# Kernel tuning notes

Hardware: AMD Instinct MI355X
Metric: run time of the kernel (lower is better)

Reference implementation:

```python
import jax, jax.numpy as jnp
import numpy as np

N_NODES = 16384
N_EDGES = 98304
N_CAND = 1024
# GAT config from default __init__: heads=[8,8,1], features=[3,64,128,64]
LAYERS = [
    (3, 8, 64, True, True),      # (f_in, n_heads, f_out, concat, elu)
    (512, 8, 128, True, True),
    (1024, 1, 64, False, False),
]


def _gat_layer(x, src, tgt, W, a_src, a_tgt, b, skipW, nh, fo, concat, act):
    n = x.shape[0]
    proj = (x @ W).reshape(n, nh, fo)                 # [N, NH, F]
    s_src = jnp.einsum('nhf,hf->nh', proj, a_src)     # [N, NH]
    s_tgt = jnp.einsum('nhf,hf->nh', proj, a_tgt)
    e = jax.nn.leaky_relu(s_src[src] + s_tgt[tgt], 0.2)   # [E, NH]
    # numerically stable segment softmax over incoming edges of each target node
    e_max = jax.ops.segment_max(e, tgt, num_segments=n)
    ex = jnp.exp(e - jax.lax.stop_gradient(e_max)[tgt])
    denom = jax.ops.segment_sum(ex, tgt, num_segments=n)
    alpha = ex / (denom[tgt] + 1e-16)                 # [E, NH]
    agg = jax.ops.segment_sum(proj[src] * alpha[:, :, None], tgt, num_segments=n)
    out = agg + (x @ skipW).reshape(n, nh, fo)        # skip connection (projected)
    out = out.reshape(n, nh * fo) if concat else out.mean(axis=1)
    out = out + b
    return jax.nn.elu(out) if act else out


def setup_inputs() -> dict:
    key = jax.random.key(0)
    ks = iter(jax.random.split(key, 32))
    d = {}
    d['fea'] = jax.random.normal(next(ks), (N_NODES, 3), dtype=jnp.float32)
    d['edge_index'] = jax.random.randint(next(ks), (2, N_EDGES), 0, N_NODES, dtype=jnp.int32)
    d['candidates_id'] = jax.random.randint(next(ks), (N_CAND,), 0, N_NODES, dtype=jnp.int32)
    for i, (fi, nh, fo, concat, _) in enumerate(LAYERS):
        sc = 1.0 / np.sqrt(fi)
        d[f'W{i}'] = jax.random.normal(next(ks), (fi, nh * fo), dtype=jnp.float32) * sc
        d[f'a_src{i}'] = jax.random.normal(next(ks), (nh, fo), dtype=jnp.float32) * 0.1
        d[f'a_tgt{i}'] = jax.random.normal(next(ks), (nh, fo), dtype=jnp.float32) * 0.1
        d[f'b{i}'] = jnp.zeros((nh * fo if concat else fo,), dtype=jnp.float32)
        d[f'skip{i}'] = jax.random.normal(next(ks), (fi, nh * fo), dtype=jnp.float32) * sc
    # MLP head build_mlp(256, 3, 64, 1): 64->256 Tanh 256->256 Tanh 256->1
    for j, (a, bdim) in enumerate([(64, 256), (256, 256), (256, 1)], start=1):
        d[f'mW{j}'] = jax.random.normal(next(ks), (a, bdim), dtype=jnp.float32) / np.sqrt(a)
        d[f'mb{j}'] = jnp.zeros((bdim,), dtype=jnp.float32)
    return d


def reference(fea, edge_index, candidates_id,
              W0, a_src0, a_tgt0, b0, skip0,
              W1, a_src1, a_tgt1, b1, skip1,
              W2, a_src2, a_tgt2, b2, skip2,
              mW1, mb1, mW2, mb2, mW3, mb3):
    src, tgt = edge_index[0], edge_index[1]
    x = fea
    params = [(W0, a_src0, a_tgt0, b0, skip0), (W1, a_src1, a_tgt1, b1, skip1),
              (W2, a_src2, a_tgt2, b2, skip2)]
    for (fi, nh, fo, concat, act), (W, asr, atg, b, sk) in zip(LAYERS, params):
        x = _gat_layer(x, src, tgt, W, asr, atg, b, sk, nh, fo, concat, act)
    cand = x[candidates_id]                              # [C, 64]
    h = jnp.tanh(cand @ mW1 + mb1)
    h = jnp.tanh(h @ mW2 + mb2)
    prob = (h @ mW3 + mb3).squeeze(-1)                   # [C]
    return prob, candidates_id
```

## Files before the change

### kernel.cpp

```cpp
#include <hip/hip_runtime.h>
#include <cmath>

#define N_NODES 16384
#define N_EDGES 98304
#define N_CAND  1024

typedef __bf16 bf16x8 __attribute__((ext_vector_type(8)));
typedef short  s16x8  __attribute__((ext_vector_type(8)));
typedef float  f32x4  __attribute__((ext_vector_type(4)));
typedef unsigned short u16x2 __attribute__((ext_vector_type(2)));
typedef unsigned short u16x4 __attribute__((ext_vector_type(4)));

__device__ __forceinline__ unsigned short f2bf(float x) {
    unsigned u = __float_as_uint(x);
    return (unsigned short)((u + 0x7fffu + ((u >> 16) & 1u)) >> 16);
}
__device__ __forceinline__ float bf2f(unsigned short b) {
    return __uint_as_float((unsigned)b << 16);
}

#define GLL(gp, lp) __builtin_amdgcn_global_load_lds(                          \
    (const __attribute__((address_space(1))) unsigned int*)(const void*)(gp),  \
    (__attribute__((address_space(3))) unsigned int*)(void*)(lp), 16, 0, 0)

__global__ __launch_bounds__(256) void k_hist(const int* __restrict__ tgt,
                                              int* __restrict__ deg) {
    int e = blockIdx.x * 256 + threadIdx.x;
    if (e < N_EDGES) atomicAdd(&deg[tgt[e]], 1);
}

__global__ __launch_bounds__(256) void k_scan_all(const int* __restrict__ deg,
                                                  int* __restrict__ off,
                                                  int* __restrict__ cursor) {
    __shared__ int ts[256];
    int tid = threadIdx.x;
    const int4* d4 = (const int4*)(deg + tid * 64);
    int s = 0;
    #pragma unroll
    for (int i = 0; i < 16; ++i) {
        int4 v = d4[i];
        s += v.x + v.y + v.z + v.w;
    }
    ts[tid] = s;
    __syncthreads();
    for (int o = 1; o < 256; o <<= 1) {
        int t = (tid >= o) ? ts[tid - o] : 0;
        __syncthreads();
        ts[tid] += t;
        __syncthreads();
    }
    int run = ts[tid] - s;
    int4* o4 = (int4*)(off + tid * 64);
    int4* c4 = (int4*)(cursor + tid * 64);
    #pragma unroll
    for (int i = 0; i < 16; ++i) {
        int4 v = d4[i];
        int4 ov;
        ov.x = run; run += v.x;
        ov.y = run; run += v.y;
        ov.z = run; run += v.z;
        ov.w = run; run += v.w;
        o4[i] = ov;
        c4[i] = ov;
    }
    if (tid == 255) off[N_NODES] = run;
}

__global__ __launch_bounds__(256) void k_scatter(const int* __restrict__ ei,
                                                 int* __restrict__ cursor,
                                                 int* __restrict__ csrc) {
    int e = blockIdx.x * 256 + threadIdx.x;
    if (e < N_EDGES) {
        int s = ei[e];
        int t = ei[N_EDGES + e];
        int pos = atomicAdd(&cursor[t], 1);
        csrc[pos] = s;
    }
}

__global__ __launch_bounds__(256) void k_l0s(const float* __restrict__ fea,
                                             const float* __restrict__ W0,
                                             const float* __restrict__ as,
                                             const float* __restrict__ at,
                                             float* __restrict__ ssrc,
                                             float* __restrict__ stgt) {
    int n = blockIdx.x, tid = threadIdx.x;
    float f0 = fea[n * 3 + 0], f1 = fea[n * 3 + 1], f2 = fea[n * 3 + 2];
    int c1 = tid, c2 = tid + 256;
    float p1 = f0 * W0[c1] + f1 * W0[512 + c1] + f2 * W0[1024 + c1];
    float p2 = f0 * W0[c2] + f1 * W0[512 + c2] + f2 * W0[1024 + c2];
    float vs1 = p1 * as[c1], vt1 = p1 * at[c1];
    float vs2 = p2 * as[c2], vt2 = p2 * at[c2];
    #pragma unroll
    for (int o = 32; o; o >>= 1) {
        vs1 += __shfl_xor(vs1, o); vt1 += __shfl_xor(vt1, o);
        vs2 += __shfl_xor(vs2, o); vt2 += __shfl_xor(vt2, o);
    }
    int lane = tid & 63, w = tid >> 6;
    if (lane == 0) {
        ssrc[n * 8 + w]     = vs1;  stgt[n * 8 + w]     = vt1;
        ssrc[n * 8 + w + 4] = vs2;  stgt[n * 8 + w + 4] = vt2;
    }
}

__device__ __forceinline__ void pack_slot(const float* __restrict__ src0,
                                          const float* __restrict__ src1,
                                          int splitN, int NTOT, int NKB, int s,
                                          unsigned short* __restrict__ hi,
                                          unsigned short* __restrict__ lo) {
    int nb = s / (NKB * 512);
    int rem = s - nb * (NKB * 512);
    int kb = rem >> 9;
    int sl = rem & 511;
    int c = sl >> 7, n = sl & 127;
    int col = nb * 128 + n;
    const float* src;
    int cc, stride;
    if (col < splitN) { src = src0; cc = col; stride = splitN; }
    else              { src = src1; cc = col - splitN; stride = NTOT - splitN; }
    int k0 = kb * 32 + c * 8;
    s16x8 hv, lv;
    #pragma unroll
    for (int j = 0; j < 8; ++j) {
        float w = src[(size_t)(k0 + j) * stride + cc];
        unsigned short h = f2bf(w);
        hv[j] = (short)h;
        lv[j] = (short)f2bf(w - bf2f(h));
    }
    *(s16x8*)(hi + (size_t)s * 8) = hv;
    *(s16x8*)(lo + (size_t)s * 8) = lv;
}

__global__ __launch_bounds__(256) void k_pack_all(
    const float* __restrict__ W1, const float* __restrict__ sk1,
    unsigned short* __restrict__ pw1h, unsigned short* __restrict__ pw1l,
    const float* __restrict__ W2, const float* __restrict__ sk2,
    unsigned short* __restrict__ pw2h, unsigned short* __restrict__ pw2l) {
    int s = blockIdx.x * 256 + threadIdx.x;
    if (s < 131072) {
        pack_slot(W1, sk1, 1024, 2048, 16, s, pw1h, pw1l);
    } else {
        int s2 = s - 131072;
        if (s2 < 16384) pack_slot(W2, sk2, 64, 128, 32, s2, pw2h, pw2l);
    }
}

template <int F, int NTOT, int KS>
__global__ __launch_bounds__(256, 2) void k_gemm_mfma(
    const unsigned short* __restrict__ Xhi, const unsigned short* __restrict__ Xlo,
    const unsigned short* __restrict__ Wph, const unsigned short* __restrict__ Wpl,
    float* __restrict__ out0, float* __restrict__ out1, int splitN) {
    constexpr int NKB = F / 32;
    static_assert(KS == 1 || NTOT == 128, "split-K assumes single col-block");
    __shared__ unsigned short lds[2 * 16384];
    const int tid = threadIdx.x;
    const int bm  = blockIdx.y * 128;
    const int nb  = blockIdx.x;

    const int sA0 = tid, sA1 = tid + 256;
    const int rA0 = sA0 >> 2, rA1 = sA1 >> 2;
    const int cA0 = (sA0 & 3) ^ ((rA0 >> 1) & 3);
    const int cA1 = (sA1 & 3) ^ ((rA1 >> 1) & 3);
    const unsigned short* gAh0 = Xhi + (size_t)(bm + rA0) * F + cA0 * 8;
    const unsigned short* gAh1 = Xhi + (size_t)(bm + rA1) * F + cA1 * 8;
    const unsigned short* gAl0 = Xlo + (size_t)(bm + rA0) * F + cA0 * 8;
    const unsigned short* gAl1 = Xlo + (size_t)(bm + rA1) * F + cA1 * 8;
    const unsigned short* gBh  = Wph + (KS == 1 ? (size_t)nb * NKB * 4096 : 0);
    const unsigned short* gBl  = Wpl + (KS == 1 ? (size_t)nb * NKB * 4096 : 0);

    const int wave = tid >> 6, lane = tid & 63;
    const int wm = wave >> 1, wn = wave & 1;
    const int l15 = lane & 15, lc = lane >> 4;

    int offA[4], offB[4];
    #pragma unroll
    for (int mi = 0; mi < 4; ++mi) {
        int row = wm * 64 + mi * 16 + l15;
        int chp = lc ^ ((row >> 1) & 3);
        offA[mi] = row * 32 + chp * 8;
    }
    #pragma unroll
    for (int ni = 0; ni < 4; ++ni) {
        int n = wn * 64 + ni * 16 + l15;
        offB[ni] = 8192 + (lc * 128 + n) * 8;
    }

    f32x4 acc[4][4];
    #pragma unroll
    for (int i = 0; i < 4; ++i)
        #pragma unroll
        for (int j = 0; j < 4; ++j)
            acc[i][j] = (f32x4){0.f, 0.f, 0.f, 0.f};

    auto stage = [&](int kb, int buf) {
        unsigned short* l = &lds[buf * 16384];
        const size_t ka  = (size_t)kb * 32;
        const size_t kbb = (size_t)kb * 4096;
        GLL(gAh0 + ka, l + sA0 * 8);
        GLL(gAh1 + ka, l + sA1 * 8);
        GLL(gAl0 + ka, l + 4096 + sA0 * 8);
        GLL(gAl1 + ka, l + 4096 + sA1 * 8);
        GLL(gBh + kbb + sA0 * 8, l + 8192 + sA0 * 8);
        GLL(gBh + kbb + sA1 * 8, l + 8192 + sA1 * 8);
        GLL(gBl + kbb + sA0 * 8, l + 12288 + sA0 * 8);
        GLL(gBl + kbb + sA1 * 8, l + 12288 + sA1 * 8);
    };

    const int kb0 = (KS > 1) ? nb * (NKB / KS) : 0;
    const int kbN = (KS > 1) ? (NKB / KS) : NKB;

    stage(kb0, 0);
    __syncthreads();

    for (int ki = 0; ki < kbN; ++ki) {
        const int buf = ki & 1;
        if (ki + 1 < kbN) stage(kb0 + ki + 1, buf ^ 1);
        const unsigned short* l = &lds[buf * 16384];
        bf16x8 ah[4], al[4], bh[4], bl[4];
        #pragma unroll
        for (int mi = 0; mi < 4; ++mi) {
            ah[mi] = *(const bf16x8*)(l + offA[mi]);
            al[mi] = *(const bf16x8*)(l + 4096 + offA[mi]);
        }
        #pragma unroll
        for (int ni = 0; ni < 4; ++ni) {
            bh[ni] = *(const bf16x8*)(l + offB[ni]);
            bl[ni] = *(const bf16x8*)(l + 4096 + offB[ni]);
        }
        #pragma unroll
        for (int mi = 0; mi < 4; ++mi)
            #pragma unroll
            for (int ni = 0; ni < 4; ++ni) {
                acc[mi][ni] = __builtin_amdgcn_mfma_f32_16x16x32_bf16(ah[mi], bh[ni], acc[mi][ni], 0, 0, 0);
                acc[mi][ni] = __builtin_amdgcn_mfma_f32_16x16x32_bf16(ah[mi], bl[ni], acc[mi][ni], 0, 0, 0);
                acc[mi][ni] = __builtin_amdgcn_mfma_f32_16x16x32_bf16(al[mi], bh[ni], acc[mi][ni], 0, 0, 0);
            }
        __syncthreads();
    }

    if constexpr (KS > 1) {
        #pragma unroll
        for (int ni = 0; ni < 4; ++ni) {
            int col = wn * 64 + ni * 16 + l15;
            #pragma unroll
            for (int mi = 0; mi < 4; ++mi) {
                int row0 = bm + wm * 64 + mi * 16 + lc * 4;
                #pragma unroll
                for (int r = 0; r < 4; ++r)
                    out0[((size_t)nb * N_NODES + row0 + r) * NTOT + col] = acc[mi][ni][r];
            }
        }
    } else {
        #pragma unroll
        for (int ni = 0; ni < 4; ++ni) {
            int col = nb * 128 + wn * 64 + ni * 16 + l15;
            float* o;
            int cc, stride;
            if (col < splitN) { o = out0; cc = col; stride = splitN; }
            else              { o = out1; cc = col - splitN; stride = NTOT - splitN; }
            #pragma unroll
            for (int mi = 0; mi < 4; ++mi) {
                int row0 = bm + wm * 64 + mi * 16 + lc * 4;
                #pragma unroll
                for (int r = 0; r < 4; ++r)
                    o[(size_t)(row0 + r) * stride + cc] = acc[mi][ni][r];
            }
        }
    }
}

__global__ __launch_bounds__(256) void k_red2s(const float* __restrict__ part,
                                               const float* __restrict__ as2,
                                               const float* __restrict__ at2,
                                               float* __restrict__ P2,
                                               float* __restrict__ S2,
                                               float* __restrict__ ssrc,
                                               float* __restrict__ stgt) {
    int tid = threadIdx.x;
    int node = blockIdx.x * 16 + (tid >> 4);
    int cg = tid & 15;
    int c0 = cg * 8;
    const float* p0 = part + (size_t)node * 128 + c0;
    float v[8];
    {
        float4 a = *(const float4*)(p0);
        float4 b = *(const float4*)(p0 + 4);
        v[0]=a.x; v[1]=a.y; v[2]=a.z; v[3]=a.w; v[4]=b.x; v[5]=b.y; v[6]=b.z; v[7]=b.w;
    }
    #pragma unroll
    for (int ks = 1; ks < 4; ++ks) {
        const float* pk = p0 + (size_t)ks * N_NODES * 128;
        float4 a = *(const float4*)(pk);
        float4 b = *(const float4*)(pk + 4);
        v[0]+=a.x; v[1]+=a.y; v[2]+=a.z; v[3]+=a.w; v[4]+=b.x; v[5]+=b.y; v[6]+=b.z; v[7]+=b.w;
    }
    if (cg < 8) {
        float s = 0.f, t = 0.f;
        #pragma unroll
        for (int j = 0; j < 8; ++j) {
            s += v[j] * as2[c0 + j];
            t += v[j] * at2[c0 + j];
        }
        #pragma unroll
        for (int o = 1; o < 8; o <<= 1) { s += __shfl_xor(s, o); t += __shfl_xor(t, o); }
        float* d = P2 + (size_t)node * 64 + c0;
        *(float4*)(d)     = make_float4(v[0], v[1], v[2], v[3]);
        *(float4*)(d + 4) = make_float4(v[4], v[5], v[6], v[7]);
        if (cg == 0) { ssrc[node] = s; stgt[node] = t; }
    } else {
        float* d = S2 + (size_t)node * 64 + (c0 - 64);
        *(float4*)(d)     = make_float4(v[0], v[1], v[2], v[3]);
        *(float4*)(d + 4) = make_float4(v[4], v[5], v[6], v[7]);
    }
}

template <int H, int FO>
__global__ __launch_bounds__(256) void k_scores(const float* __restrict__ P,
                                                const float* __restrict__ asrc,
                                                const float* __restrict__ atgt,
                                                float* __restrict__ ssrc,
                                                float* __restrict__ stgt) {
    constexpr int K = H * FO;
    int gid  = blockIdx.x * 4 + (threadIdx.x >> 6);
    int lane = threadIdx.x & 63;
    int n = gid / H, h = gid - n * H;
    if (n >= N_NODES) return;
    float vs = 0.f, vt = 0.f;
    #pragma unroll
    for (int q = 0; q < FO / 64; ++q) {
        int f = lane + q * 64;
        float p = P[(size_t)n * K + h * FO + f];
        vs += p * asrc[h * FO + f];
        vt += p * atgt[h * FO + f];
    }
    #pragma unroll
    for (int o = 32; o; o >>= 1) {
        vs += __shfl_xor(vs, o);
        vt += __shfl_xor(vt, o);
    }
    if (lane == 0) {
        ssrc[n * H + h] = vs;
        stgt[n * H + h] = vt;
    }
}

__global__ __launch_bounds__(256) void k_attn0(
    const float* __restrict__ fea, const float* __restrict__ W0,
    const float* __restrict__ sk0, const float* __restrict__ ssrc,
    const float* __restrict__ stgt, const int* __restrict__ off,
    const int* __restrict__ csrc, const float* __restrict__ bias,
    unsigned short* __restrict__ ohi, unsigned short* __restrict__ olo) {
    constexpr int H = 8, K = 512;
    int n = blockIdx.x, tid = threadIdx.x;
    __shared__ float st[H], mh[H], dh[H];
    __shared__ int   srcs[256];
    __shared__ float sfea[256][3];
    __shared__ float av[256 * H];
    const int c0 = tid * 2, h0 = tid >> 5;

    float w00 = W0[c0],        w01 = W0[c0 + 1];
    float w10 = W0[512 + c0],  w11 = W0[512 + c0 + 1];
    float w20 = W0[1024 + c0], w21 = W0[1024 + c0 + 1];

    int d0 = off[n], deg = off[n + 1] - d0;
    if (tid < H) st[tid] = stgt[n * H + tid];
    __syncthreads();

    float a0 = 0.f, a1 = 0.f;

    if (deg <= 256) {
        int cnt = deg;
        if (tid < cnt) srcs[tid] = csrc[d0 + tid];
        __syncthreads();
        for (int idx = tid; idx < cnt * 3; idx += 256)
            sfea[idx / 3][idx % 3] = fea[srcs[idx / 3] * 3 + idx % 3];
        for (int idx = tid; idx < cnt * H; idx += 256) {
            int e = idx >> 3, h = idx & 7;
            float v = ssrc[srcs[e] * H + h] + st[h];
            av[idx] = (v >= 0.f) ? v : 0.2f * v;
        }
        __syncthreads();
        if (tid < H) {
            float m = -INFINITY;
            for (int e = 0; e < cnt; ++e) m = fmaxf(m, av[e * H + tid]);
            float s = 0.f;
            for (int e = 0; e < cnt; ++e) s += expf(av[e * H + tid] - m);
            mh[tid] = m;
            dh[tid] = 1.f / (s + 1e-16f);
        }
        __syncthreads();
        for (int idx = tid; idx < cnt * H; idx += 256) {
            int h = idx & 7;
            av[idx] = expf(av[idx] - mh[h]) * dh[h];
        }
        __syncthreads();
        for (int e = 0; e < cnt; ++e) {
            float al = av[e * H + h0];
            float f0 = sfea[e][0], f1 = sfea[e][1], f2 = sfea[e][2];
            a0 += (f0 * w00 + f1 * w10 + f2 * w20) * al;
            a1 += (f0 * w01 + f1 * w11 + f2 * w21) * al;
        }
    } else {
        if (tid < H) { mh[tid] = -INFINITY; dh[tid] = 0.f; }
        __syncthreads();
        for (int base = 0; base < deg; base += 256) {
            int cnt = min(256, deg - base);
            if (tid < cnt) srcs[tid] = csrc[d0 + base + tid];
            __syncthreads();
            for (int idx = tid; idx < cnt * H; idx += 256) {
                int e = idx >> 3, h = idx & 7;
                float v = ssrc[srcs[e] * H + h] + st[h];
                av[idx] = (v >= 0.f) ? v : 0.2f * v;
            }
            __syncthreads();
            if (tid < H) {
                float m = mh[tid], d = dh[tid];
                float cm = -INFINITY;
                for (int e = 0; e < cnt; ++e) cm = fmaxf(cm, av[e * H + tid]);
                float nm = fmaxf(m, cm);
                float s = 0.f;
                for (int e = 0; e < cnt; ++e) s += expf(av[e * H + tid] - nm);
                d = ((m == -INFINITY) ? 0.f : d * expf(m - nm)) + s;
                mh[tid] = nm;
                dh[tid] = d;
            }
            __syncthreads();
        }
        if (tid < H) dh[tid] = 1.f / (dh[tid] + 1e-16f);
        __syncthreads();
        for (int base = 0; base < deg; base += 256) {
            int cnt = min(256, deg - base);
            if (tid < cnt) srcs[tid] = csrc[d0 + base + tid];
            __syncthreads();
            for (int idx = tid; idx < cnt * 3; idx += 256)
                sfea[idx / 3][idx % 3] = fea[srcs[idx / 3] * 3 + idx % 3];
            for (int idx = tid; idx < cnt * H; idx += 256) {
                int e = idx >> 3, h = idx & 7;
                float v = ssrc[srcs[e] * H + h] + st[h];
                v = (v >= 0.f) ? v : 0.2f * v;
                av[idx] = expf(v - mh[h]) * dh[h];
            }
            __syncthreads();
            for (int e = 0; e < cnt; ++e) {
                float al = av[e * H + h0];
                float f0 = sfea[e][0], f1 = sfea[e][1], f2 = sfea[e][2];
                a0 += (f0 * w00 + f1 * w10 + f2 * w20) * al;
                a1 += (f0 * w01 + f1 * w11 + f2 * w21) * al;
            }
            __syncthreads();
        }
    }

    float f0 = fea[n * 3], f1 = fea[n * 3 + 1], f2 = fea[n * 3 + 2];
    float r0 = a0 + f0 * sk0[c0]     + f1 * sk0[512 + c0]     + f2 * sk0[1024 + c0]     + bias[c0];
    float r1 = a1 + f0 * sk0[c0 + 1] + f1 * sk0[512 + c0 + 1] + f2 * sk0[1024 + c0 + 1] + bias[c0 + 1];
    r0 = (r0 > 0.f) ? r0 : expm1f(r0);
    r1 = (r1 > 0.f) ? r1 : expm1f(r1);
    u16x2 hv, lv;
    unsigned short hb0 = f2bf(r0); hv[0] = hb0; lv[0] = f2bf(r0 - bf2f(hb0));
    unsigned short hb1 = f2bf(r1); hv[1] = hb1; lv[1] = f2bf(r1 - bf2f(hb1));
    *(u16x2*)(ohi + (size_t)n * K + c0) = hv;
    *(u16x2*)(olo + (size_t)n * K + c0) = lv;
}

template <int H, int FO, bool ACT, bool SPLIT>
__global__ __launch_bounds__(256) void k_attn_g(
    const float* __restrict__ P, const float* __restrict__ ssrc,
    const float* __restrict__ stgt, const int* __restrict__ off,
    const int* __restrict__ csrc, const float* __restrict__ bias,
    const float* __restrict__ skipin, float* __restrict__ outf,
    unsigned short* __restrict__ ohi, unsigned short* __restrict__ olo) {
    constexpr int K   = H * FO;
    constexpr int VEC = (K / 256 >= 4) ? 4 : ((K / 256 >= 1) ? (K / 256) : 1);
    constexpr int NT  = K / VEC;
    int n = blockIdx.x, tid = threadIdx.x;
    __shared__ float st[H], mh[H], dh[H];
    __shared__ int   srcs[256];
    __shared__ float av[256 * H];

    const int c0 = (tid < NT ? tid : 0) * VEC;
    const int h0 = c0 / FO;
    const float* pc = P + c0;

    int d0 = off[n], deg = off[n + 1] - d0;
    if (tid < H) st[tid] = stgt[n * H + tid];
    __syncthreads();

    float acc[VEC];
    #pragma unroll
    for (int j = 0; j < VEC; ++j) acc[j] = 0.f;

    if (deg <= 256) {
        int cnt = deg;
        if (tid < cnt) srcs[tid] = csrc[d0 + tid];
        __syncthreads();
        for (int idx = tid; idx < cnt * H; idx += 256) {
            int e = idx / H, h = idx - (idx / H) * H;
            float v = ssrc[srcs[e] * H + h] + st[h];
            av[idx] = (v >= 0.f) ? v : 0.2f * v;
        }
        __syncthreads();
        if (tid < H) {
            float m = -INFINITY;
            for (int e = 0; e < cnt; ++e) m = fmaxf(m, av[e * H + tid]);
            float s = 0.f;
            for (int e = 0; e < cnt; ++e) s += expf(av[e * H + tid] - m);
            mh[tid] = m;
            dh[tid] = 1.f / (s + 1e-16f);
        }
        __syncthreads();
        for (int idx = tid; idx < cnt * H; idx += 256) {
            int h = idx - (idx / H) * H;
            av[idx] = expf(av[idx] - mh[h]) * dh[h];
        }
        __syncthreads();
        if (NT == 256 || tid < NT) {
            for (int e = 0; e < cnt; ++e) {
                float a = av[e * H + h0];
                if constexpr (VEC == 4) {
                    const float4 v = *(const float4*)(pc + (size_t)srcs[e] * K);
                    acc[0] += v.x * a; acc[1] += v.y * a;
                    acc[2] += v.z * a; acc[3] += v.w * a;
                } else {
                    acc[0] += pc[(size_t)srcs[e] * K] * a;
                }
            }
        }
    } else {
        if (tid < H) { mh[tid] = -INFINITY; dh[tid] = 0.f; }
        __syncthreads();
        for (int base = 0; base < deg; base += 256) {
            int cnt = min(256, deg - base);
            if (tid < cnt) srcs[tid] = csrc[d0 + base + tid];
            __syncthreads();
            for (int idx = tid; idx < cnt * H; idx += 256) {
                int e = idx / H, h = idx - (idx / H) * H;
                float v = ssrc[srcs[e] * H + h] + st[h];
                av[idx] = (v >= 0.f) ? v : 0.2f * v;
            }
            __syncthreads();
            if (tid < H) {
                float m = mh[tid], d = dh[tid];
                float cm = -INFINITY;
                for (int e = 0; e < cnt; ++e) cm = fmaxf(cm, av[e * H + tid]);
                float nm = fmaxf(m, cm);
                float s = 0.f;
                for (int e = 0; e < cnt; ++e) s += expf(av[e * H + tid] - nm);
                d = ((m == -INFINITY) ? 0.f : d * expf(m - nm)) + s;
                mh[tid] = nm;
                dh[tid] = d;
            }
            __syncthreads();
        }
        if (tid < H) dh[tid] = 1.f / (dh[tid] + 1e-16f);
        __syncthreads();
        for (int base = 0; base < deg; base += 256) {
            int cnt = min(256, deg - base);
            if (tid < cnt) srcs[tid] = csrc[d0 + base + tid];
            __syncthreads();
            for (int idx = tid; idx < cnt * H; idx += 256) {
                int e = idx / H, h = idx - (idx / H) * H;
                float v = ssrc[srcs[e] * H + h] + st[h];
                v = (v >= 0.f) ? v : 0.2f * v;
                av[idx] = expf(v - mh[h]) * dh[h];
            }
            __syncthreads();
            if (NT == 256 || tid < NT) {
                for (int e = 0; e < cnt; ++e) {
                    float a = av[e * H + h0];
                    if constexpr (VEC == 4) {
                        const float4 v = *(const float4*)(pc + (size_t)srcs[e] * K);
                        acc[0] += v.x * a; acc[1] += v.y * a;
                        acc[2] += v.z * a; acc[3] += v.w * a;
                    } else {
                        acc[0] += pc[(size_t)srcs[e] * K] * a;
                    }
                }
            }
            __syncthreads();
        }
    }

    if (NT == 256 || tid < NT) {
        float r[VEC];
        if constexpr (VEC == 4) {
            const float4 s4 = *(const float4*)(skipin + (size_t)n * K + c0);
            r[0] = acc[0] + s4.x; r[1] = acc[1] + s4.y;
            r[2] = acc[2] + s4.z; r[3] = acc[3] + s4.w;
        } else {
            r[0] = acc[0] + skipin[(size_t)n * K + c0];
        }
        #pragma unroll
        for (int j = 0; j < VEC; ++j) {
            r[j] += bias[c0 + j];
            if (ACT) r[j] = (r[j] > 0.f) ? r[j] : expm1f(r[j]);
        }
        if constexpr (SPLIT) {
            if constexpr (VEC == 4) {
                u16x4 hv, lv;
                #pragma unroll
                for (int j = 0; j < 4; ++j) {
                    unsigned short hb = f2bf(r[j]);
                    hv[j] = hb; lv[j] = f2bf(r[j] - bf2f(hb));
                }
                *(u16x4*)(ohi + (size_t)n * K + c0) = hv;
                *(u16x4*)(olo + (size_t)n * K + c0) = lv;
            } else {
                unsigned short hb = f2bf(r[0]);
                ohi[(size_t)n * K + c0] = hb;
                olo[(size_t)n * K + c0] = f2bf(r[0] - bf2f(hb));
            }
        } else {
            if constexpr (VEC == 4) {
                *(float4*)(outf + (size_t)n * K + c0) =
                    make_float4(r[0], r[1], r[2], r[3]);
            } else {
                outf[(size_t)n * K + c0] = r[0];
            }
        }
    }
}

__global__ __launch_bounds__(256) void k_mlp(const float* __restrict__ X3,
                                             const int* __restrict__ cid,
                                             const float* __restrict__ W1,
                                             const float* __restrict__ b1,
                                             const float* __restrict__ W2,
                                             const float* __restrict__ b2,
                                             const float* __restrict__ W3,
                                             const float* __restrict__ b3,
                                             float* __restrict__ out) {
    __shared__ float cf[64], h1[256], red[4];
    int c = blockIdx.x, tid = threadIdx.x;
    int id = cid[c];
    if (tid < 64) cf[tid] = X3[(size_t)id * 64 + tid];
    __syncthreads();
    float a = b1[tid];
    #pragma unroll 8
    for (int k = 0; k < 64; ++k) a += cf[k] * W1[k * 256 + tid];
    h1[tid] = tanhf(a);
    __syncthreads();
    float a2 = b2[tid];
    #pragma unroll 8
    for (int k = 0; k < 256; ++k) a2 += h1[k] * W2[k * 256 + tid];
    float v = tanhf(a2) * W3[tid];
    #pragma unroll
    for (int o = 32; o; o >>= 1) v += __shfl_xor(v, o);
    if ((tid & 63) == 0) red[tid >> 6] = v;
    __syncthreads();
    if (tid == 0) {
        out[c] = red[0] + red[1] + red[2] + red[3] + b3[0];
        out[N_CAND + c] = (float)id;
    }
}

extern "C" void kernel_launch(void* const* d_in, const int* in_sizes, int n_in,
                              void* d_out, int out_size, void* d_ws, size_t ws_size,
                              hipStream_t stream) {
    const float* fea  = (const float*)d_in[0];
    const int*   ei   = (const int*)d_in[1];
    const int*   cid  = (const int*)d_in[2];
    const float* W0   = (const float*)d_in[3];
    const float* as0  = (const float*)d_in[4];
    const float* at0  = (const float*)d_in[5];
    const float* b0   = (const float*)d_in[6];
    const float* sk0  = (const float*)d_in[7];
    const float* W1   = (const float*)d_in[8];
    const float* as1  = (const float*)d_in[9];
    const float* at1  = (const float*)d_in[10];
    const float* b1   = (const float*)d_in[11];
    const float* sk1  = (const float*)d_in[12];
    const float* W2   = (const float*)d_in[13];
    const float* as2  = (const float*)d_in[14];
    const float* at2  = (const float*)d_in[15];
    const float* b2   = (const float*)d_in[16];
    const float* sk2  = (const float*)d_in[17];
    const float* mW1  = (const float*)d_in[18];
    const float* mb1  = (const float*)d_in[19];
    const float* mW2  = (const float*)d_in[20];
    const float* mb2  = (const float*)d_in[21];
    const float* mW3  = (const float*)d_in[22];
    const float* mb3  = (const float*)d_in[23];

    char* w = (char*)d_ws;
    auto alloc = [&](size_t bytes) -> void* {
        void* p = (void*)w;
        w += (bytes + 255) & ~(size_t)255;
        return p;
    };
    int*   deg    = (int*)alloc((size_t)N_NODES * 4);
    int*   off    = (int*)alloc((size_t)(N_NODES + 1) * 4);
    int*   cursor = (int*)alloc((size_t)N_NODES * 4);
    int*   csrc   = (int*)alloc((size_t)N_EDGES * 4);
    float* ssrc   = (float*)alloc((size_t)N_NODES * 8 * 4);
    float* stgt   = (float*)alloc((size_t)N_NODES * 8 * 4);
    float* P      = (float*)alloc((size_t)N_NODES * 1024 * 4);
    float* S      = (float*)alloc((size_t)N_NODES * 1024 * 4);
    unsigned short* Xs = (unsigned short*)alloc((size_t)N_NODES * 1024 * 4);
    unsigned short* pw1h = (unsigned short*)alloc((size_t)512 * 2048 * 2);
    unsigned short* pw1l = (unsigned short*)alloc((size_t)512 * 2048 * 2);
    unsigned short* pw2h = (unsigned short*)alloc((size_t)1024 * 128 * 2);
    unsigned short* pw2l = (unsigned short*)alloc((size_t)1024 * 128 * 2);

    unsigned short* X1hi = Xs;
    unsigned short* X1lo = Xs + (size_t)N_NODES * 512;
    unsigned short* X2hi = Xs;
    unsigned short* X2lo = Xs + (size_t)N_NODES * 1024;
    float* part = P;
    float* P2   = S;
    float* S2   = S + (size_t)N_NODES * 64;
    float* X3   = S + (size_t)2 * N_NODES * 64;

    hipMemsetAsync(deg, 0, (size_t)N_NODES * 4, stream);
    k_hist<<<N_EDGES / 256, 256, 0, stream>>>(ei + N_EDGES, deg);
    k_scan_all<<<1, 256, 0, stream>>>(deg, off, cursor);
    k_scatter<<<N_EDGES / 256, 256, 0, stream>>>(ei, cursor, csrc);

    k_pack_all<<<576, 256, 0, stream>>>(W1, sk1, pw1h, pw1l, W2, sk2, pw2h, pw2l);

    k_l0s<<<N_NODES, 256, 0, stream>>>(fea, W0, as0, at0, ssrc, stgt);
    k_attn0<<<N_NODES, 256, 0, stream>>>(fea, W0, sk0, ssrc, stgt, off, csrc,
                                         b0, X1hi, X1lo);

    {
        dim3 g(16, N_NODES / 128);
        k_gemm_mfma<512, 2048, 1><<<g, 256, 0, stream>>>(X1hi, X1lo, pw1h, pw1l, P, S, 1024);
    }
    k_scores<8, 128><<<N_NODES * 8 / 4, 256, 0, stream>>>(P, as1, at1, ssrc, stgt);
    k_attn_g<8, 128, true, true><<<N_NODES, 256, 0, stream>>>(
        P, ssrc, stgt, off, csrc, b1, S, nullptr, X2hi, X2lo);

    {
        dim3 g(4, N_NODES / 128);
        k_gemm_mfma<1024, 128, 4><<<g, 256, 0, stream>>>(X2hi, X2lo, pw2h, pw2l, part, nullptr, 128);
    }
    k_red2s<<<N_NODES / 16, 256, 0, stream>>>(part, as2, at2, P2, S2, ssrc, stgt);
    k_attn_g<1, 64, false, false><<<N_NODES, 256, 0, stream>>>(
        P2, ssrc, stgt, off, csrc, b2, S2, X3, nullptr, nullptr);

    k_mlp<<<N_CAND, 256, 0, stream>>>(X3, cid, mW1, mb1, mW2, mb2, mW3, mb3,
                                      (float*)d_out);
}
```

Measured before the change: 468.4 us.

## Fuse layer-1 scores into GEMM epilogue, compute last layer only for candidates, batch MLP

The layer-1 attention score dot products move into the MFMA GEMM epilogue, which removes the separate k_scores kernel and its re-read of the 16384x1024 projection. The final GAT layer's aggregation now runs only for the 1024 candidate nodes instead of all 16384, because only those rows are consumed by the MLP. The MLP kernel is batched to process 16 candidates per block, so W1 and W2 loads are reused across candidates. The costs are extra LDS use and a sync in the GEMM epilogue, plus higher register pressure in the MLP.

```diff
diff --git a/kernel.cpp b/kernel.cpp
--- a/kernel.cpp
+++ b/kernel.cpp
@@ -145,11 +145,13 @@
     }
 }
 
-template <int F, int NTOT, int KS>
+template <int F, int NTOT, int KS, bool FS>
 __global__ __launch_bounds__(256, 2) void k_gemm_mfma(
     const unsigned short* __restrict__ Xhi, const unsigned short* __restrict__ Xlo,
     const unsigned short* __restrict__ Wph, const unsigned short* __restrict__ Wpl,
-    float* __restrict__ out0, float* __restrict__ out1, int splitN) {
+    float* __restrict__ out0, float* __restrict__ out1, int splitN,
+    const float* __restrict__ as, const float* __restrict__ at,
+    float* __restrict__ ssrc, float* __restrict__ stgt) {
     constexpr int NKB = F / 32;
     static_assert(KS == 1 || NTOT == 128, "split-K assumes single col-block");
     __shared__ unsigned short lds[2 * 16384];
@@ -264,6 +266,44 @@
                 #pragma unroll
                 for (int r = 0; r < 4; ++r)
                     o[(size_t)(row0 + r) * stride + cc] = acc[mi][ni][r];
+            }
+        }
+        if constexpr (FS) {
+            if (nb < 8) {
+                float* sredS = (float*)lds;
+                float* sredT = sredS + 256;
+                const float* av_ = as + nb * 128;
+                const float* atv = at + nb * 128;
+                #pragma unroll
+                for (int mi = 0; mi < 4; ++mi) {
+                    #pragma unroll
+                    for (int r = 0; r < 4; ++r) {
+                        float ps = 0.f, pt = 0.f;
+                        #pragma unroll
+                        for (int ni = 0; ni < 4; ++ni) {
+                            int f = wn * 64 + ni * 16 + l15;
+                            float v = acc[mi][ni][r];
+                            ps += v * av_[f];
+                            pt += v * atv[f];
+                        }
+                        #pragma unroll
+                        for (int o = 1; o < 16; o <<= 1) {
+                            ps += __shfl_xor(ps, o);
+                            pt += __shfl_xor(pt, o);
+                        }
+                        if (l15 == 0) {
+                            int rl = wm * 64 + mi * 16 + lc * 4 + r;
+                            sredS[wn * 128 + rl] = ps;
+                            sredT[wn * 128 + rl] = pt;
+                        }
+                    }
+                }
+                __syncthreads();
+                if (tid < 128) {
+                    int row = bm + tid;
+                    ssrc[row * 8 + nb] = sredS[tid] + sredS[128 + tid];
+                    stgt[row * 8 + nb] = sredT[tid] + sredT[128 + tid];
+                }
             }
         }
     }
@@ -314,36 +354,6 @@
     }
 }
 
-template <int H, int FO>
-__global__ __launch_bounds__(256) void k_scores(const float* __restrict__ P,
-                                                const float* __restrict__ asrc,
-                                                const float* __restrict__ atgt,
-                                                float* __restrict__ ssrc,
-                                                float* __restrict__ stgt) {
-    constexpr int K = H * FO;
-    int gid  = blockIdx.x * 4 + (threadIdx.x >> 6);
-    int lane = threadIdx.x & 63;
-    int n = gid / H, h = gid - n * H;
-    if (n >= N_NODES) return;
-    float vs = 0.f, vt = 0.f;
-    #pragma unroll
-    for (int q = 0; q < FO / 64; ++q) {
-        int f = lane + q * 64;
-        float p = P[(size_t)n * K + h * FO + f];
-        vs += p * asrc[h * FO + f];
-        vt += p * atgt[h * FO + f];
-    }
-    #pragma unroll
-    for (int o = 32; o; o >>= 1) {
-        vs += __shfl_xor(vs, o);
-        vt += __shfl_xor(vt, o);
-    }
-    if (lane == 0) {
-        ssrc[n * H + h] = vs;
-        stgt[n * H + h] = vt;
-    }
-}
-
 __global__ __launch_bounds__(256) void k_attn0(
     const float* __restrict__ fea, const float* __restrict__ W0,
     const float* __restrict__ sk0, const float* __restrict__ ssrc,
@@ -463,17 +473,20 @@
     *(u16x2*)(olo + (size_t)n * K + c0) = lv;
 }
 
-template <int H, int FO, bool ACT, bool SPLIT>
+template <int H, int FO, bool ACT, bool SPLIT, bool CAND>
 __global__ __launch_bounds__(256) void k_attn_g(
     const float* __restrict__ P, const float* __restrict__ ssrc,
     const float* __restrict__ stgt, const int* __restrict__ off,
     const int* __restrict__ csrc, const float* __restrict__ bias,
     const float* __restrict__ skipin, float* __restrict__ outf,
-    unsigned short* __restrict__ ohi, unsigned short* __restrict__ olo) {
+    unsigned short* __restrict__ ohi, unsigned short* __restrict__ olo,
+    const int* __restrict__ nidx) {
     constexpr int K   = H * FO;
     constexpr int VEC = (K / 256 >= 4) ? 4 : ((K / 256 >= 1) ? (K / 256) : 1);
     constexpr int NT  = K / VEC;
-    int n = blockIdx.x, tid = threadIdx.x;
+    int n = CAND ? nidx[blockIdx.x] : blockIdx.x;
+    int orow = CAND ? blockIdx.x : n;
+    int tid = threadIdx.x;
     __shared__ float st[H], mh[H], dh[H];
     __shared__ int   srcs[256];
     __shared__ float av[256 * H];
@@ -603,25 +616,25 @@
                     unsigned short hb = f2bf(r[j]);
                     hv[j] = hb; lv[j] = f2bf(r[j] - bf2f(hb));
                 }
-                *(u16x4*)(ohi + (size_t)n * K + c0) = hv;
-                *(u16x4*)(olo + (size_t)n * K + c0) = lv;
+                *(u16x4*)(ohi + (size_t)orow * K + c0) = hv;
+                *(u16x4*)(olo + (size_t)orow * K + c0) = lv;
             } else {
                 unsigned short hb = f2bf(r[0]);
-                ohi[(size_t)n * K + c0] = hb;
-                olo[(size_t)n * K + c0] = f2bf(r[0] - bf2f(hb));
+                ohi[(size_t)orow * K + c0] = hb;
+                olo[(size_t)orow * K + c0] = f2bf(r[0] - bf2f(hb));
             }
         } else {
             if constexpr (VEC == 4) {
-                *(float4*)(outf + (size_t)n * K + c0) =
+                *(float4*)(outf + (size_t)orow * K + c0) =
                     make_float4(r[0], r[1], r[2], r[3]);
             } else {
-                outf[(size_t)n * K + c0] = r[0];
-            }
-        }
-    }
-}
-
-__global__ __launch_bounds__(256) void k_mlp(const float* __restrict__ X3,
+                outf[(size_t)orow * K + c0] = r[0];
+            }
+        }
+    }
+}
+
+__global__ __launch_bounds__(256) void k_mlp(const float* __restrict__ X3c,
                                              const int* __restrict__ cid,
                                              const float* __restrict__ W1,
                                              const float* __restrict__ b1,
@@ -630,27 +643,46 @@
                                              const float* __restrict__ W3,
                                              const float* __restrict__ b3,
                                              float* __restrict__ out) {
-    __shared__ float cf[64], h1[256], red[4];
-    int c = blockIdx.x, tid = threadIdx.x;
-    int id = cid[c];
-    if (tid < 64) cf[tid] = X3[(size_t)id * 64 + tid];
+    __shared__ float cf[16][64];
+    __shared__ float h1s[16][256];
+    __shared__ float red[16][4];
+    int tid = threadIdx.x;
+    int cbase = blockIdx.x * 16;
+    for (int i = tid; i < 16 * 64; i += 256)
+        cf[i >> 6][i & 63] = X3c[(size_t)cbase * 64 + i];
     __syncthreads();
-    float a = b1[tid];
-    #pragma unroll 8
-    for (int k = 0; k < 64; ++k) a += cf[k] * W1[k * 256 + tid];
-    h1[tid] = tanhf(a);
+    float a[16];
+    #pragma unroll
+    for (int ci = 0; ci < 16; ++ci) a[ci] = b1[tid];
+    for (int k = 0; k < 64; ++k) {
+        float wv = W1[k * 256 + tid];
+        #pragma unroll
+        for (int ci = 0; ci < 16; ++ci) a[ci] += cf[ci][k] * wv;
+    }
+    #pragma unroll
+    for (int ci = 0; ci < 16; ++ci) h1s[ci][tid] = tanhf(a[ci]);
     __syncthreads();
-    float a2 = b2[tid];
-    #pragma unroll 8
-    for (int k = 0; k < 256; ++k) a2 += h1[k] * W2[k * 256 + tid];
-    float v = tanhf(a2) * W3[tid];
-    #pragma unroll
-    for (int o = 32; o; o >>= 1) v += __shfl_xor(v, o);
-    if ((tid & 63) == 0) red[tid >> 6] = v;
+    #pragma unroll
+    for (int ci = 0; ci < 16; ++ci) a[ci] = b2[tid];
+    for (int k = 0; k < 256; ++k) {
+        float wv = W2[k * 256 + tid];
+        #pragma unroll
+        for (int ci = 0; ci < 16; ++ci) a[ci] += h1s[ci][k] * wv;
+    }
+    float w3 = W3[tid];
+    int lane = tid & 63, wv_ = tid >> 6;
+    #pragma unroll
+    for (int ci = 0; ci < 16; ++ci) {
+        float v = tanhf(a[ci]) * w3;
+        #pragma unroll
+        for (int o = 32; o; o >>= 1) v += __shfl_xor(v, o);
+        if (lane == 0) red[ci][wv_] = v;
+    }
     __syncthreads();
-    if (tid == 0) {
-        out[c] = red[0] + red[1] + red[2] + red[3] + b3[0];
-        out[N_CAND + c] = (float)id;
+    if (tid < 16) {
+        int c = cbase + tid;
+        out[c] = red[tid][0] + red[tid][1] + red[tid][2] + red[tid][3] + b3[0];
+        out[N_CAND + c] = (float)cid[c];
     }
 }
 
@@ -709,7 +741,7 @@
     float* part = P;
     float* P2   = S;
     float* S2   = S + (size_t)N_NODES * 64;
-    float* X3   = S + (size_t)2 * N_NODES * 64;
+    float* X3c  = S + (size_t)2 * N_NODES * 64;
 
     hipMemsetAsync(deg, 0, (size_t)N_NODES * 4, stream);
     k_hist<<<N_EDGES / 256, 256, 0, stream>>>(ei + N_EDGES, deg);
@@ -724,20 +756,22 @@
 
     {
         dim3 g(16, N_NODES / 128);
-        k_gemm_mfma<512, 2048, 1><<<g, 256, 0, stream>>>(X1hi, X1lo, pw1h, pw1l, P, S, 1024);
-    }
-    k_scores<8, 128><<<N_NODES * 8 / 4, 256, 0, stream>>>(P, as1, at1, ssrc, stgt);
-    k_attn_g<8, 128, true, true><<<N_NODES, 256, 0, stream>>>(
-        P, ssrc, stgt, off, csrc, b1, S, nullptr, X2hi, X2lo);
+        k_gemm_mfma<512, 2048, 1, true><<<g, 256, 0, stream>>>(
+            X1hi, X1lo, pw1h, pw1l, P, S, 1024, as1, at1, ssrc, stgt);
+    }
+    k_attn_g<8, 128, true, true, false><<<N_NODES, 256, 0, stream>>>(
+        P, ssrc, stgt, off, csrc, b1, S, nullptr, X2hi, X2lo, nullptr);
 
     {
         dim3 g(4, N_NODES / 128);
-        k_gemm_mfma<1024, 128, 4><<<g, 256, 0, stream>>>(X2hi, X2lo, pw2h, pw2l, part, nullptr, 128);
+        k_gemm_mfma<1024, 128, 4, false><<<g, 256, 0, stream>>>(
+            X2hi, X2lo, pw2h, pw2l, part, nullptr, 128,
+            nullptr, nullptr, nullptr, nullptr);
     }
     k_red2s<<<N_NODES / 16, 256, 0, stream>>>(part, as2, at2, P2, S2, ssrc, stgt);
-    k_attn_g<1, 64, false, false><<<N_NODES, 256, 0, stream>>>(
-        P2, ssrc, stgt, off, csrc, b2, S2, X3, nullptr, nullptr);
-
-    k_mlp<<<N_CAND, 256, 0, stream>>>(X3, cid, mW1, mb1, mW2, mb2, mW3, mb3,
-                                      (float*)d_out);
-}
+    k_attn_g<1, 64, false, false, true><<<N_CAND, 256, 0, stream>>>(
+        P2, ssrc, stgt, off, csrc, b2, S2, X3c, nullptr, nullptr, cid);
+
+    k_mlp<<<N_CAND / 16, 256, 0, stream>>>(X3c, cid, mW1, mb1, mW2, mb2, mW3, mb3,
+                                           (float*)d_out);
+}
```

New measurement: 466.7 us. Within noise of the previous version (-0.4%).
